# Performance work log

Hardware: AMD Instinct MI355X
Metric: run time of the kernel (lower is better)

Reference implementation:

```python
import jax, jax.numpy as jnp
import numpy as np

N_NODES = 100_000
N_EDGES = 1_600_000
NUM_GRAPHS = 512
D1, D2, D3, D5, NUM_CLASSES = 3, 50, 15, 10, 6
BN_EPS = 1e-5


def setup_inputs() -> dict:
    key = jax.random.key(0)
    ks = jax.random.split(key, 16)

    def w(k, shape):
        fan_in = shape[0]
        return jax.random.normal(k, shape, jnp.float32) / np.sqrt(fan_in).astype(np.float32)

    return {
        "x": jax.random.normal(ks[0], (N_NODES, D1), jnp.float32),
        "edge_attr": jax.random.normal(ks[1], (N_EDGES, D1), jnp.float32),
        # edge MLP: Lin(9,50) -> ReLU -> Lin(50,15)
        "edge_w1": w(ks[2], (3 * D1, D2)), "edge_b1": jnp.zeros((D2,), jnp.float32),
        "edge_w2": w(ks[3], (D2, D3)), "edge_b2": jnp.zeros((D3,), jnp.float32),
        # node MLP: Lin(18,50) -> ReLU -> Lin(50,15)
        "node_w1": w(ks[4], (D1 + D3, D2)), "node_b1": jnp.zeros((D2,), jnp.float32),
        "node_w2": w(ks[5], (D2, D3)), "node_b2": jnp.zeros((D3,), jnp.float32),
        # readout head
        "fc1_w": w(ks[6], (D3, D5)), "fc1_b": jnp.zeros((D5,), jnp.float32),
        "bn_gamma": jnp.ones((D5,), jnp.float32), "bn_beta": jnp.zeros((D5,), jnp.float32),
        "fc2_w": w(ks[7], (D5, NUM_CLASSES)), "fc2_b": jnp.zeros((NUM_CLASSES,), jnp.float32),
        # graph structure
        "edge_index": jax.random.randint(ks[8], (2, N_EDGES), 0, N_NODES, jnp.int32),
        "batch": jnp.sort(jax.random.randint(ks[9], (N_NODES,), 0, NUM_GRAPHS, jnp.int32)),
    }


def _segment_mean(vals, idx, num_segments):
    s = jax.ops.segment_sum(vals, idx, num_segments=num_segments)
    c = jax.ops.segment_sum(jnp.ones((vals.shape[0], 1), vals.dtype), idx,
                            num_segments=num_segments)
    return s / jnp.maximum(c, 1.0)


def reference(x, edge_attr,
              edge_w1, edge_b1, edge_w2, edge_b2,
              node_w1, node_b1, node_w2, node_b2,
              fc1_w, fc1_b, bn_gamma, bn_beta, fc2_w, fc2_b,
              edge_index, batch):
    row, col = edge_index[0], edge_index[1]
    # edge model: cat([x[row], x[col], edge_attr]) -> MLP  -> [E, D3]
    e_in = jnp.concatenate([x[row], x[col], edge_attr], axis=1)
    edge_attr2 = jax.nn.relu(e_in @ edge_w1 + edge_b1) @ edge_w2 + edge_b2
    # node model: cat([x[col], edge_attr2]) -> MLP -> scatter_mean over row
    n_in = jnp.concatenate([x[col], edge_attr2], axis=1)  # [E, D1+D3]
    msg = jax.nn.relu(n_in @ node_w1 + node_b1) @ node_w2 + node_b2  # [E, D3]
    x2 = _segment_mean(msg, row, x.shape[0])  # [N, D3]
    # global mean pool per graph -> [G, D3]
    u = _segment_mean(x2, batch, NUM_GRAPHS)
    # head: fc1 -> BatchNorm1d (batch stats) -> relu -> fc2 -> log_softmax
    h = u @ fc1_w + fc1_b
    mu = h.mean(axis=0)
    var = h.var(axis=0)  # biased, matches BN training normalization
    h = bn_gamma * (h - mu) * jax.lax.rsqrt(var + BN_EPS) + bn_beta
    h = jax.nn.relu(h)
    logits = h @ fc2_w + fc2_b
    return jax.nn.log_softmax(logits, axis=1)
```

## Files before the change

kernel.cpp:

```cpp
#include <hip/hip_runtime.h>
#include <hip/hip_bf16.h>
#include <math.h>

#define N_NODES    100000
#define N_EDGES    1600000
#define NUM_GRAPHS 512
#define D2 50
#define D3 15
#define D5 10
#define NCLS 6
#define BN_EPS 1e-5f

#define NBLK1 ((N_NODES + 1023) / 1024)

#define W_EW1T 0
#define W_EW2T 2560
#define W_NW1T 3712
#define W_NW2T 6272
#define W_TOTAL 7680

#define EDGE_BLOCKS 2500
#define EDGE_WAVES  (EDGE_BLOCKS * 4)
#define TILES32     (N_EDGES / 32)
#define EDGE_ITERS  (TILES32 / EDGE_WAVES)

typedef __attribute__((ext_vector_type(8))) short short8;
typedef __attribute__((ext_vector_type(4))) float float4_;
union BU { unsigned u[4]; short8 s; };
union FU { unsigned u; float f; };

__device__ __forceinline__ unsigned short f2bf(float f) {
    __hip_bfloat16 h = __float2bfloat16(f);
    union { __hip_bfloat16 h; unsigned short u; } c; c.h = h; return c.u;
}
__device__ __forceinline__ unsigned pkbf(float a, float b) {
    unsigned r;
    asm("v_cvt_pk_bf16_f32 %0, %1, %2" : "=v"(r) : "v"(a), "v"(b));
    return r;
}
__device__ __forceinline__ unsigned bp(int s4, unsigned v) {
    return (unsigned)__builtin_amdgcn_ds_bpermute(s4, (int)v);
}
__device__ __forceinline__ float lo16(unsigned u) { FU c; c.u = u << 16; return c.f; }
__device__ __forceinline__ float hi16(unsigned u) { FU c; c.u = u & 0xFFFF0000u; return c.f; }

__global__ __launch_bounds__(256) void prep_kernel(
    const float* __restrict__ ew1, const float* __restrict__ eb1,
    const float* __restrict__ ew2, const float* __restrict__ eb2,
    const float* __restrict__ nw1, const float* __restrict__ nb1,
    const float* __restrict__ nw2, const float* __restrict__ nb2,
    unsigned short* __restrict__ wh,
    const float* __restrict__ x, ushort4* __restrict__ x4b,
    const int* __restrict__ edge_index, int* __restrict__ counts)
{
    int gtid = blockIdx.x * 256 + threadIdx.x;
    int gsz = gridDim.x * 256;

    for (int i = gtid; i < W_TOTAL; i += gsz) {
        float v = 0.0f;
        if (i < W_EW2T) {
            int m = i / 40, k = i % 40;
            if (m < 50) {
                if (k < 3)                 v = ew1[k * 50 + m];
                else if (k == 3)           v = eb1[m];
                else if (k >= 4 && k < 7)  v = ew1[(k - 1) * 50 + m];
                else if (k >= 8 && k < 11) v = ew1[(k - 2) * 50 + m];
            }
        } else if (i < W_NW1T) {
            int j = i - W_EW2T; int m = j / 72, k = j % 72;
            if (m < 15) { if (k < 50) v = ew2[k * 15 + m]; else if (k == 50) v = eb2[m]; }
        } else if (i < W_NW2T) {
            int j = i - W_NW1T; int m = j / 40, k = j % 40;
            if (m < 50) {
                if (k < 15)                  v = nw1[(3 + k) * 50 + m];
                else if (k >= 16 && k < 19)  v = nw1[(k - 16) * 50 + m];
                else if (k == 19)            v = nb1[m];
            }
        } else if (i < 7424) {
            int j = i - W_NW2T; int m = j / 72, k = j % 72;
            if (m < 15) { if (k < 50) v = nw2[k * 15 + m]; else if (k == 50) v = nb2[m]; }
        }
        wh[i] = f2bf(v);
    }

    for (int n = gtid; n < N_NODES; n += gsz) {
        ushort4 v;
        v.x = f2bf(x[n * 3 + 0]); v.y = f2bf(x[n * 3 + 1]);
        v.z = f2bf(x[n * 3 + 2]); v.w = 0;
        x4b[n] = v;
    }

    for (int e = gtid; e < N_EDGES; e += gsz)
        atomicAdd(&counts[edge_index[e]], 1);
}

__global__ __launch_bounds__(1024) void scan_kernel(
    const int* __restrict__ counts, int* __restrict__ scanned,
    int* __restrict__ cursor, int* __restrict__ gctr)
{
    __shared__ int wsum[16], wofs[16];
    __shared__ int base;
    int i = blockIdx.x * 1024 + threadIdx.x;
    int lane = threadIdx.x & 63, wid = threadIdx.x >> 6;
    int v = (i < N_NODES) ? counts[i] : 0;
    int sc = v;
    #pragma unroll
    for (int off = 1; off < 64; off <<= 1) {
        int t = __shfl_up(sc, off);
        if (lane >= off) sc += t;
    }
    if (lane == 63) wsum[wid] = sc;
    __syncthreads();
    if (wid == 0) {
        int s = (lane < 16) ? wsum[lane] : 0;
        #pragma unroll
        for (int off = 1; off < 16; off <<= 1) {
            int t = __shfl_up(s, off);
            if (lane >= off) s += t;
        }
        if (lane < 16) wofs[lane] = s - wsum[lane];
    }
    __syncthreads();
    int incl = sc + wofs[wid];
    if (threadIdx.x == 1023) base = atomicAdd(gctr, incl);
    __syncthreads();
    int start = base + incl - v;
    if (i < N_NODES) { scanned[i] = start; cursor[i] = start; }
}

struct EIn { unsigned w0, w1, w2, w3, h0, h1; int pos; };

__device__ __forceinline__ EIn load_in(int ebase, int n, int quad,
    const int* __restrict__ edge_index, const ushort4* __restrict__ x4b,
    const float* __restrict__ edge_attr, int* __restrict__ cursor)
{
    EIn r; r.w0 = r.w1 = r.w2 = r.w3 = 0; r.h0 = r.h1 = 0; r.pos = 0;
    int e = ebase + n;
    if (quad == 0) {
        int row = edge_index[e];
        int col = edge_index[N_EDGES + e];
        ushort4 xr = x4b[row];
        ushort4 xc = x4b[col];
        r.w0 = (unsigned)xr.x | ((unsigned)xr.y << 16);
        r.w1 = (unsigned)xr.z | (0x3F80u << 16);
        r.w2 = (unsigned)xc.x | ((unsigned)xc.y << 16);
        r.w3 = (unsigned)xc.z;
        r.pos = atomicAdd(&cursor[row], 1);
    } else if (quad == 1) {
        r.w0 = pkbf(edge_attr[e * 3 + 0], edge_attr[e * 3 + 1]);
        r.w1 = pkbf(edge_attr[e * 3 + 2], 0.0f);
    } else if (quad == 2) {
        int col = edge_index[N_EDGES + e];
        ushort4 xc = x4b[col];
        r.h0 = (unsigned)xc.x | ((unsigned)xc.y << 16);
        r.h1 = (unsigned)xc.z | (0x3F80u << 16);
    }
    return r;
}

__device__ __forceinline__ void perm64(const unsigned U[4][2], int s0, int s1, bool hi,
                                       short8& Bc0, short8& Bc1)
{
    BU b0, b1;
    {
        unsigned a0 = bp(s0, U[0][0]), a1 = bp(s0, U[1][0]);
        unsigned a2 = bp(s0, U[0][1]), a3 = bp(s0, U[1][1]);
        unsigned a4 = bp(s1, U[0][0]), a5 = bp(s1, U[1][0]);
        unsigned a6 = bp(s1, U[0][1]), a7 = bp(s1, U[1][1]);
        b0.u[0] = hi ? a1 : a0;
        b0.u[1] = hi ? a3 : a2;
        b0.u[2] = hi ? a5 : a4;
        b0.u[3] = hi ? a7 : a6;
    }
    {
        unsigned a0 = bp(s0, U[2][0]), a1 = bp(s0, U[3][0]);
        unsigned a2 = bp(s0, U[2][1]), a3 = bp(s0, U[3][1]);
        unsigned a4 = bp(s1, U[2][0]), a5 = bp(s1, U[3][0]);
        unsigned a6 = bp(s1, U[2][1]), a7 = bp(s1, U[3][1]);
        b1.u[0] = hi ? a1 : a0;
        b1.u[1] = hi ? a3 : a2;
        b1.u[2] = hi ? a5 : a4;
        b1.u[3] = hi ? a7 : a6;
    }
    Bc0 = b0.s; Bc1 = b1.s;
}

__device__ __forceinline__ short8 perm16(const unsigned U2[2], int s0, int s1,
                                         int quad, unsigned h0, unsigned h1)
{
    BU d;
    d.u[0] = bp(s0, U2[0]);
    d.u[1] = bp(s0, U2[1]);
    d.u[2] = bp(s1, U2[0]);
    d.u[3] = bp(s1, U2[1]);
    if (quad == 2) { d.u[0] = h0; d.u[1] = h1; d.u[2] = 0; d.u[3] = 0; }
    else if (quad == 3) { d.u[0] = 0; d.u[1] = 0; d.u[2] = 0; d.u[3] = 0; }
    return d.s;
}

__global__ __launch_bounds__(256) void edge_mfma_kernel(
    const unsigned short* __restrict__ wh_g,
    const ushort4* __restrict__ x4b, const float* __restrict__ edge_attr,
    const int* __restrict__ edge_index,
    int* __restrict__ cursor, unsigned short* __restrict__ msgb)
{
    int tid = threadIdx.x, wave = tid >> 6, lane = tid & 63;
    int n = lane & 15, quad = lane >> 4;

    short8 A1[4], A3[4];
    #pragma unroll
    for (int t4 = 0; t4 < 4; t4++) {
        A1[t4] = *(const short8*)(wh_g + W_EW1T + (t4 * 16 + n) * 40 + quad * 8);
        A3[t4] = *(const short8*)(wh_g + W_NW1T + (t4 * 16 + n) * 40 + quad * 8);
    }
    short8 A2[2], A4[2];
    #pragma unroll
    for (int kc = 0; kc < 2; kc++) {
        A2[kc] = *(const short8*)(wh_g + W_EW2T + n * 72 + kc * 32 + quad * 8);
        A4[kc] = *(const short8*)(wh_g + W_NW2T + n * 72 + kc * 32 + quad * 8);
    }

    int s0 = ((quad & 1) * 32 + n) * 4;
    int s1 = s0 + 64;
    bool hi = (quad & 2) != 0;

    const float4_ Z0 = {0.f, 0.f, 0.f, 0.f};

    int t = blockIdx.x * 4 + wave;
    EIn cur0 = load_in(t * 32,      n, quad, edge_index, x4b, edge_attr, cursor);
    EIn cur1 = load_in(t * 32 + 16, n, quad, edge_index, x4b, edge_attr, cursor);

    for (int it = 0; it < EDGE_ITERS; it++) {
        int p0 = __shfl(cur0.pos, n);
        int p1 = __shfl(cur1.pos, n);

        int tn = t + EDGE_WAVES;
        EIn nx0, nx1;
        nx0.w0 = nx0.w1 = nx0.w2 = nx0.w3 = nx0.h0 = nx0.h1 = 0; nx0.pos = 0;
        nx1 = nx0;
        if (it + 1 < EDGE_ITERS) {
            nx0 = load_in(tn * 32,      n, quad, edge_index, x4b, edge_attr, cursor);
            nx1 = load_in(tn * 32 + 16, n, quad, edge_index, x4b, edge_attr, cursor);
        }

        BU t0, t1;
        t0.u[0] = cur0.w0; t0.u[1] = cur0.w1; t0.u[2] = cur0.w2; t0.u[3] = cur0.w3;
        t1.u[0] = cur1.w0; t1.u[1] = cur1.w1; t1.u[2] = cur1.w2; t1.u[3] = cur1.w3;
        short8 B1a = t0.s, B1b = t1.s;

        unsigned U1a[4][2], U1b[4][2];
        #pragma unroll
        for (int t4 = 0; t4 < 4; t4++) {
            float4_ za = __builtin_amdgcn_mfma_f32_16x16x32_bf16(A1[t4], B1a, Z0, 0, 0, 0);
            float4_ zb = __builtin_amdgcn_mfma_f32_16x16x32_bf16(A1[t4], B1b, Z0, 0, 0, 0);
            U1a[t4][0] = pkbf(fmaxf(za[0], 0.f), fmaxf(za[1], 0.f));
            U1a[t4][1] = pkbf(fmaxf(za[2], 0.f), fmaxf(za[3], 0.f));
            U1b[t4][0] = pkbf(fmaxf(zb[0], 0.f), fmaxf(zb[1], 0.f));
            U1b[t4][1] = pkbf(fmaxf(zb[2], 0.f), fmaxf(zb[3], 0.f));
        }

        short8 B2a0, B2a1, B2b0, B2b1;
        perm64(U1a, s0, s1, hi, B2a0, B2a1);
        perm64(U1b, s0, s1, hi, B2b0, B2b1);
        if (quad == 2) {
            BU fa, fb; fa.s = B2a1; fb.s = B2b1;
            fa.u[1] = (fa.u[1] & 0xFFFF0000u) | 0x3F80u;
            fb.u[1] = (fb.u[1] & 0xFFFF0000u) | 0x3F80u;
            B2a1 = fa.s; B2b1 = fb.s;
        }

        float4_ a2a = __builtin_amdgcn_mfma_f32_16x16x32_bf16(A2[0], B2a0, Z0, 0, 0, 0);
        float4_ a2b = __builtin_amdgcn_mfma_f32_16x16x32_bf16(A2[0], B2b0, Z0, 0, 0, 0);
        a2a = __builtin_amdgcn_mfma_f32_16x16x32_bf16(A2[1], B2a1, a2a, 0, 0, 0);
        a2b = __builtin_amdgcn_mfma_f32_16x16x32_bf16(A2[1], B2b1, a2b, 0, 0, 0);

        unsigned U2a[2] = { pkbf(a2a[0], a2a[1]), pkbf(a2a[2], a2a[3]) };
        unsigned U2b[2] = { pkbf(a2b[0], a2b[1]), pkbf(a2b[2], a2b[3]) };

        short8 B3a = perm16(U2a, s0, s1, quad, cur0.h0, cur0.h1);
        short8 B3b = perm16(U2b, s0, s1, quad, cur1.h0, cur1.h1);

        unsigned U3a[4][2], U3b[4][2];
        #pragma unroll
        for (int t4 = 0; t4 < 4; t4++) {
            float4_ za = __builtin_amdgcn_mfma_f32_16x16x32_bf16(A3[t4], B3a, Z0, 0, 0, 0);
            float4_ zb = __builtin_amdgcn_mfma_f32_16x16x32_bf16(A3[t4], B3b, Z0, 0, 0, 0);
            U3a[t4][0] = pkbf(fmaxf(za[0], 0.f), fmaxf(za[1], 0.f));
            U3a[t4][1] = pkbf(fmaxf(za[2], 0.f), fmaxf(za[3], 0.f));
            U3b[t4][0] = pkbf(fmaxf(zb[0], 0.f), fmaxf(zb[1], 0.f));
            U3b[t4][1] = pkbf(fmaxf(zb[2], 0.f), fmaxf(zb[3], 0.f));
        }

        short8 B4a0, B4a1, B4b0, B4b1;
        perm64(U3a, s0, s1, hi, B4a0, B4a1);
        perm64(U3b, s0, s1, hi, B4b0, B4b1);
        if (quad == 2) {
            BU fa, fb; fa.s = B4a1; fb.s = B4b1;
            fa.u[1] = (fa.u[1] & 0xFFFF0000u) | 0x3F80u;
            fb.u[1] = (fb.u[1] & 0xFFFF0000u) | 0x3F80u;
            B4a1 = fa.s; B4b1 = fb.s;
        }

        float4_ ma = __builtin_amdgcn_mfma_f32_16x16x32_bf16(A4[0], B4a0, Z0, 0, 0, 0);
        float4_ mb = __builtin_amdgcn_mfma_f32_16x16x32_bf16(A4[0], B4b0, Z0, 0, 0, 0);
        ma = __builtin_amdgcn_mfma_f32_16x16x32_bf16(A4[1], B4a1, ma, 0, 0, 0);
        mb = __builtin_amdgcn_mfma_f32_16x16x32_bf16(A4[1], B4b1, mb, 0, 0, 0);

        uint2 pa, pb;
        pa.x = pkbf(ma[0], ma[1]); pa.y = pkbf(ma[2], ma[3]);
        pb.x = pkbf(mb[0], mb[1]); pb.y = pkbf(mb[2], mb[3]);
        *(uint2*)(msgb + (size_t)p0 * 16 + quad * 4) = pa;
        *(uint2*)(msgb + (size_t)p1 * 16 + quad * 4) = pb;

        cur0 = nx0; cur1 = nx1; t = tn;
    }
}

__global__ __launch_bounds__(256) void gather_pool_kernel(
    const unsigned short* __restrict__ msgb, const int* __restrict__ scanned,
    const int* __restrict__ counts, const int* __restrict__ batch,
    float* __restrict__ gsum)
{
    __shared__ float acc[64 * 16];
    int n0 = blockIdx.x * 256;
    int n = n0 + threadIdx.x;

    float v[16];
    #pragma unroll
    for (int k = 0; k < 16; k++) v[k] = 0.0f;
    if (n < N_NODES) {
        int start = scanned[n];
        int deg = counts[n];
        const uint4* mp = (const uint4*)(msgb + (size_t)start * 16);
        int j = 0;
        for (; j + 4 <= deg; j += 4) {
            uint4 q0 = mp[2 * j + 0], q1 = mp[2 * j + 1];
            uint4 q2 = mp[2 * j + 2], q3 = mp[2 * j + 3];
            uint4 q4 = mp[2 * j + 4], q5 = mp[2 * j + 5];
            uint4 q6 = mp[2 * j + 6], q7 = mp[2 * j + 7];
            v[0]  += lo16(q0.x) + lo16(q2.x) + lo16(q4.x) + lo16(q6.x);
            v[1]  += hi16(q0.x) + hi16(q2.x) + hi16(q4.x) + hi16(q6.x);
            v[2]  += lo16(q0.y) + lo16(q2.y) + lo16(q4.y) + lo16(q6.y);
            v[3]  += hi16(q0.y) + hi16(q2.y) + hi16(q4.y) + hi16(q6.y);
            v[4]  += lo16(q0.z) + lo16(q2.z) + lo16(q4.z) + lo16(q6.z);
            v[5]  += hi16(q0.z) + hi16(q2.z) + hi16(q4.z) + hi16(q6.z);
            v[6]  += lo16(q0.w) + lo16(q2.w) + lo16(q4.w) + lo16(q6.w);
            v[7]  += hi16(q0.w) + hi16(q2.w) + hi16(q4.w) + hi16(q6.w);
            v[8]  += lo16(q1.x) + lo16(q3.x) + lo16(q5.x) + lo16(q7.x);
            v[9]  += hi16(q1.x) + hi16(q3.x) + hi16(q5.x) + hi16(q7.x);
            v[10] += lo16(q1.y) + lo16(q3.y) + lo16(q5.y) + lo16(q7.y);
            v[11] += hi16(q1.y) + hi16(q3.y) + hi16(q5.y) + hi16(q7.y);
            v[12] += lo16(q1.z) + lo16(q3.z) + lo16(q5.z) + lo16(q7.z);
            v[13] += hi16(q1.z) + hi16(q3.z) + hi16(q5.z) + hi16(q7.z);
            v[14] += lo16(q1.w) + lo16(q3.w) + lo16(q5.w) + lo16(q7.w);
        }
        for (; j < deg; j++) {
            uint4 qa = mp[2 * j + 0], qb = mp[2 * j + 1];
            v[0]  += lo16(qa.x); v[1]  += hi16(qa.x);
            v[2]  += lo16(qa.y); v[3]  += hi16(qa.y);
            v[4]  += lo16(qa.z); v[5]  += hi16(qa.z);
            v[6]  += lo16(qa.w); v[7]  += hi16(qa.w);
            v[8]  += lo16(qb.x); v[9]  += hi16(qb.x);
            v[10] += lo16(qb.y); v[11] += hi16(qb.y);
            v[12] += lo16(qb.z); v[13] += hi16(qb.z);
            v[14] += lo16(qb.w);
        }
        float inv = 1.0f / fmaxf((float)deg, 1.0f);
        #pragma unroll
        for (int k = 0; k < 15; k++) v[k] *= inv;
        v[15] = 1.0f;
    }

    int gmin = batch[n0];
    int gmax = batch[min(n0 + 255, N_NODES - 1)];
    int range = gmax - gmin + 1;
    if (range <= 64) {
        for (int t = threadIdx.x; t < range * 16; t += 256) acc[t] = 0.0f;
        __syncthreads();
        if (n < N_NODES) {
            int g = batch[n] - gmin;
            float* dst = &acc[g * 16];
            #pragma unroll
            for (int k = 0; k < 16; k++) atomicAdd(&dst[k], v[k]);
        }
        __syncthreads();
        for (int t = threadIdx.x; t < range * 16; t += 256) {
            float w = acc[t];
            if (w != 0.0f) atomicAdd(&gsum[(size_t)gmin * 16 + t], w);
        }
    } else {
        if (n < N_NODES) {
            int g = batch[n];
            float* dst = gsum + (size_t)g * 16;
            #pragma unroll
            for (int k = 0; k < 16; k++) atomicAdd(&dst[k], v[k]);
        }
    }
}

__global__ __launch_bounds__(512) void head_kernel(
    const float* __restrict__ gsum,
    const float* __restrict__ fc1w, const float* __restrict__ fc1b,
    const float* __restrict__ gamma, const float* __restrict__ beta,
    const float* __restrict__ fc2w, const float* __restrict__ fc2b,
    float* __restrict__ out)
{
    __shared__ float ssum[D5], ssq[D5], smu[D5], sistd[D5];
    int g = threadIdx.x;
    if (g < D5) { ssum[g] = 0.0f; ssq[g] = 0.0f; }
    __syncthreads();

    const float* src = gsum + (size_t)g * 16;
    float inv = 1.0f / fmaxf(src[15], 1.0f);
    float u[D3];
    #pragma unroll
    for (int k = 0; k < D3; k++) u[k] = src[k] * inv;

    float h[D5];
    #pragma unroll
    for (int c = 0; c < D5; c++) h[c] = fc1b[c];
    #pragma unroll
    for (int k = 0; k < D3; k++) {
        float v = u[k];
        #pragma unroll
        for (int c = 0; c < D5; c++) h[c] = fmaf(v, fc1w[k * D5 + c], h[c]);
    }

    int lane = threadIdx.x & 63;
    #pragma unroll
    for (int c = 0; c < D5; c++) {
        float v = h[c];
        float v2 = v * v;
        #pragma unroll
        for (int off = 32; off >= 1; off >>= 1) {
            v  += __shfl_xor(v,  off);
            v2 += __shfl_xor(v2, off);
        }
        if (lane == 0) { atomicAdd(&ssum[c], v); atomicAdd(&ssq[c], v2); }
    }
    __syncthreads();
    if (g < D5) {
        float mu = ssum[g] * (1.0f / NUM_GRAPHS);
        float var = ssq[g] * (1.0f / NUM_GRAPHS) - mu * mu;
        smu[g] = mu;
        sistd[g] = rsqrtf(var + BN_EPS);
    }
    __syncthreads();

    float hn[D5];
    #pragma unroll
    for (int c = 0; c < D5; c++) {
        float v = gamma[c] * (h[c] - smu[c]) * sistd[c] + beta[c];
        hn[c] = fmaxf(v, 0.0f);
    }

    float lg[NCLS];
    #pragma unroll
    for (int j = 0; j < NCLS; j++) lg[j] = fc2b[j];
    #pragma unroll
    for (int c = 0; c < D5; c++) {
        float v = hn[c];
        #pragma unroll
        for (int j = 0; j < NCLS; j++) lg[j] = fmaf(v, fc2w[c * NCLS + j], lg[j]);
    }

    float m = lg[0];
    #pragma unroll
    for (int j = 1; j < NCLS; j++) m = fmaxf(m, lg[j]);
    float se = 0.0f;
    #pragma unroll
    for (int j = 0; j < NCLS; j++) se += expf(lg[j] - m);
    float lse = logf(se);
    #pragma unroll
    for (int j = 0; j < NCLS; j++) out[g * NCLS + j] = lg[j] - m - lse;
}

extern "C" void kernel_launch(void* const* d_in, const int* in_sizes, int n_in,
                              void* d_out, int out_size, void* d_ws, size_t ws_size,
                              hipStream_t stream) {
    const float* x         = (const float*)d_in[0];
    const float* edge_attr = (const float*)d_in[1];
    const float* ew1  = (const float*)d_in[2];
    const float* eb1  = (const float*)d_in[3];
    const float* ew2  = (const float*)d_in[4];
    const float* eb2  = (const float*)d_in[5];
    const float* nw1  = (const float*)d_in[6];
    const float* nb1  = (const float*)d_in[7];
    const float* nw2  = (const float*)d_in[8];
    const float* nb2  = (const float*)d_in[9];
    const float* fc1w = (const float*)d_in[10];
    const float* fc1b = (const float*)d_in[11];
    const float* gamma= (const float*)d_in[12];
    const float* beta = (const float*)d_in[13];
    const float* fc2w = (const float*)d_in[14];
    const float* fc2b = (const float*)d_in[15];
    const int* edge_index = (const int*)d_in[16];
    const int* batch      = (const int*)d_in[17];

    char* p = (char*)d_ws;
    unsigned short* msgb = (unsigned short*)p; p += (size_t)N_EDGES * 16 * sizeof(unsigned short);
    int* counts  = (int*)p;            p += (size_t)N_NODES * sizeof(int);
    int* gctr    = (int*)p;            p += 4 * sizeof(int);
    int* scanned = (int*)p;            p += (size_t)N_NODES * sizeof(int);
    int* cursor  = (int*)p;            p += (size_t)N_NODES * sizeof(int);
    ushort4* x4b = (ushort4*)p;        p += (size_t)N_NODES * sizeof(ushort4);
    float* gsum  = (float*)p;          p += (size_t)NUM_GRAPHS * 16 * sizeof(float);
    unsigned short* wh = (unsigned short*)p; p += W_TOTAL * sizeof(unsigned short);

    hipMemsetAsync(counts, 0, (size_t)(N_NODES + 4) * sizeof(int), stream);
    hipMemsetAsync(gsum, 0, (size_t)NUM_GRAPHS * 16 * sizeof(float), stream);

    int egrid = (N_EDGES + 255) / 256;
    int ngrid = (N_NODES + 255) / 256;

    prep_kernel<<<egrid, 256, 0, stream>>>(
        ew1, eb1, ew2, eb2, nw1, nb1, nw2, nb2, wh,
        x, x4b, edge_index, counts);
    scan_kernel<<<NBLK1, 1024, 0, stream>>>(counts, scanned, cursor, gctr);
    edge_mfma_kernel<<<EDGE_BLOCKS, 256, 0, stream>>>(
        wh, x4b, edge_attr, edge_index, cursor, msgb);
    gather_pool_kernel<<<ngrid, 256, 0, stream>>>(
        msgb, scanned, counts, batch, gsum);
    head_kernel<<<1, 512, 0, stream>>>(
        gsum, fc1w, fc1b, gamma, beta, fc2w, fc2b, (float*)d_out);
}
```

Baseline: 312.5 us.

## Fuse edge MLP with per-graph pooling via 1/deg-weighted shared-memory accumulation

The change removes the CSR scan, the per-edge message buffer and the gather kernel. Each edge message is scaled by 1/deg(row) and added straight into a per-block shared-memory accumulator indexed by graph id, which works because the mean-of-means is linear. Per-block partials (1024×512×16 floats) are written out and summed by a new reduce kernel. Node counts per graph are now computed in prep through a shared histogram. This saves the write and read of the 51 MB bf16 message buffer and the scan launch. In exchange it adds many LDS float atomics per edge and roughly 32 MB of partial writes and reads.

```diff
diff --git a/kernel.cpp b/kernel.cpp
--- a/kernel.cpp
+++ b/kernel.cpp
@@ -11,23 +11,21 @@
 #define NCLS 6
 #define BN_EPS 1e-5f
 
-#define NBLK1 ((N_NODES + 1023) / 1024)
-
 #define W_EW1T 0
 #define W_EW2T 2560
 #define W_NW1T 3712
 #define W_NW2T 6272
 #define W_TOTAL 7680
 
-#define EDGE_BLOCKS 2500
+#define EDGE_BLOCKS 1024
 #define EDGE_WAVES  (EDGE_BLOCKS * 4)
 #define TILES32     (N_EDGES / 32)
-#define EDGE_ITERS  (TILES32 / EDGE_WAVES)
+
+#define GPAD 17
 
 typedef __attribute__((ext_vector_type(8))) short short8;
 typedef __attribute__((ext_vector_type(4))) float float4_;
 union BU { unsigned u[4]; short8 s; };
-union FU { unsigned u; float f; };
 
 __device__ __forceinline__ unsigned short f2bf(float f) {
     __hip_bfloat16 h = __float2bfloat16(f);
@@ -41,8 +39,6 @@
 __device__ __forceinline__ unsigned bp(int s4, unsigned v) {
     return (unsigned)__builtin_amdgcn_ds_bpermute(s4, (int)v);
 }
-__device__ __forceinline__ float lo16(unsigned u) { FU c; c.u = u << 16; return c.f; }
-__device__ __forceinline__ float hi16(unsigned u) { FU c; c.u = u & 0xFFFF0000u; return c.f; }
 
 __global__ __launch_bounds__(256) void prep_kernel(
     const float* __restrict__ ew1, const float* __restrict__ eb1,
@@ -51,10 +47,15 @@
     const float* __restrict__ nw2, const float* __restrict__ nb2,
     unsigned short* __restrict__ wh,
     const float* __restrict__ x, ushort4* __restrict__ x4b,
-    const int* __restrict__ edge_index, int* __restrict__ counts)
-{
+    const int* __restrict__ edge_index, int* __restrict__ counts,
+    const int* __restrict__ batch, float* __restrict__ gsum)
+{
+    __shared__ int bh[NUM_GRAPHS];
     int gtid = blockIdx.x * 256 + threadIdx.x;
     int gsz = gridDim.x * 256;
+
+    for (int i = threadIdx.x; i < NUM_GRAPHS; i += 256) bh[i] = 0;
+    __syncthreads();
 
     for (int i = gtid; i < W_TOTAL; i += gsz) {
         float v = 0.0f;
@@ -88,53 +89,27 @@
         v.x = f2bf(x[n * 3 + 0]); v.y = f2bf(x[n * 3 + 1]);
         v.z = f2bf(x[n * 3 + 2]); v.w = 0;
         x4b[n] = v;
+        atomicAdd(&bh[batch[n]], 1);
     }
 
     for (int e = gtid; e < N_EDGES; e += gsz)
         atomicAdd(&counts[edge_index[e]], 1);
-}
-
-__global__ __launch_bounds__(1024) void scan_kernel(
-    const int* __restrict__ counts, int* __restrict__ scanned,
-    int* __restrict__ cursor, int* __restrict__ gctr)
-{
-    __shared__ int wsum[16], wofs[16];
-    __shared__ int base;
-    int i = blockIdx.x * 1024 + threadIdx.x;
-    int lane = threadIdx.x & 63, wid = threadIdx.x >> 6;
-    int v = (i < N_NODES) ? counts[i] : 0;
-    int sc = v;
-    #pragma unroll
-    for (int off = 1; off < 64; off <<= 1) {
-        int t = __shfl_up(sc, off);
-        if (lane >= off) sc += t;
-    }
-    if (lane == 63) wsum[wid] = sc;
-    __syncthreads();
-    if (wid == 0) {
-        int s = (lane < 16) ? wsum[lane] : 0;
-        #pragma unroll
-        for (int off = 1; off < 16; off <<= 1) {
-            int t = __shfl_up(s, off);
-            if (lane >= off) s += t;
-        }
-        if (lane < 16) wofs[lane] = s - wsum[lane];
-    }
-    __syncthreads();
-    int incl = sc + wofs[wid];
-    if (threadIdx.x == 1023) base = atomicAdd(gctr, incl);
-    __syncthreads();
-    int start = base + incl - v;
-    if (i < N_NODES) { scanned[i] = start; cursor[i] = start; }
-}
-
-struct EIn { unsigned w0, w1, w2, w3, h0, h1; int pos; };
+
+    __syncthreads();
+    for (int i = threadIdx.x; i < NUM_GRAPHS; i += 256) {
+        int v = bh[i];
+        if (v) atomicAdd(&gsum[i * 16 + 15], (float)v);
+    }
+}
+
+struct EIn { unsigned w0, w1, w2, w3, h0, h1; int g; float invd; };
 
 __device__ __forceinline__ EIn load_in(int ebase, int n, int quad,
     const int* __restrict__ edge_index, const ushort4* __restrict__ x4b,
-    const float* __restrict__ edge_attr, int* __restrict__ cursor)
-{
-    EIn r; r.w0 = r.w1 = r.w2 = r.w3 = 0; r.h0 = r.h1 = 0; r.pos = 0;
+    const float* __restrict__ edge_attr,
+    const int* __restrict__ counts, const int* __restrict__ batch)
+{
+    EIn r; r.w0 = r.w1 = r.w2 = r.w3 = 0; r.h0 = r.h1 = 0; r.g = 0; r.invd = 0.0f;
     int e = ebase + n;
     if (quad == 0) {
         int row = edge_index[e];
@@ -145,7 +120,8 @@
         r.w1 = (unsigned)xr.z | (0x3F80u << 16);
         r.w2 = (unsigned)xc.x | ((unsigned)xc.y << 16);
         r.w3 = (unsigned)xc.z;
-        r.pos = atomicAdd(&cursor[row], 1);
+        r.g = batch[row];
+        r.invd = 1.0f / (float)counts[row];
     } else if (quad == 1) {
         r.w0 = pkbf(edge_attr[e * 3 + 0], edge_attr[e * 3 + 1]);
         r.w1 = pkbf(edge_attr[e * 3 + 2], 0.0f);
@@ -198,14 +174,19 @@
     return d.s;
 }
 
-__global__ __launch_bounds__(256) void edge_mfma_kernel(
+__global__ __launch_bounds__(256) void edge_fused_kernel(
     const unsigned short* __restrict__ wh_g,
     const ushort4* __restrict__ x4b, const float* __restrict__ edge_attr,
     const int* __restrict__ edge_index,
-    int* __restrict__ cursor, unsigned short* __restrict__ msgb)
-{
+    const int* __restrict__ counts, const int* __restrict__ batch,
+    float* __restrict__ partial)
+{
+    __shared__ float acc[NUM_GRAPHS * GPAD];
     int tid = threadIdx.x, wave = tid >> 6, lane = tid & 63;
     int n = lane & 15, quad = lane >> 4;
+
+    for (int i = tid; i < NUM_GRAPHS * GPAD; i += 256) acc[i] = 0.0f;
+    __syncthreads();
 
     short8 A1[4], A3[4];
     #pragma unroll
@@ -227,20 +208,23 @@
     const float4_ Z0 = {0.f, 0.f, 0.f, 0.f};
 
     int t = blockIdx.x * 4 + wave;
-    EIn cur0 = load_in(t * 32,      n, quad, edge_index, x4b, edge_attr, cursor);
-    EIn cur1 = load_in(t * 32 + 16, n, quad, edge_index, x4b, edge_attr, cursor);
-
-    for (int it = 0; it < EDGE_ITERS; it++) {
-        int p0 = __shfl(cur0.pos, n);
-        int p1 = __shfl(cur1.pos, n);
+    EIn cur0 = load_in(t * 32,      n, quad, edge_index, x4b, edge_attr, counts, batch);
+    EIn cur1 = load_in(t * 32 + 16, n, quad, edge_index, x4b, edge_attr, counts, batch);
+
+    for (;;) {
+        int g0 = __shfl(cur0.g, n);
+        float q0 = __shfl(cur0.invd, n);
+        int g1 = __shfl(cur1.g, n);
+        float q1 = __shfl(cur1.invd, n);
 
         int tn = t + EDGE_WAVES;
+        bool more = (tn < TILES32);
         EIn nx0, nx1;
-        nx0.w0 = nx0.w1 = nx0.w2 = nx0.w3 = nx0.h0 = nx0.h1 = 0; nx0.pos = 0;
+        nx0.w0 = nx0.w1 = nx0.w2 = nx0.w3 = nx0.h0 = nx0.h1 = 0; nx0.g = 0; nx0.invd = 0.f;
         nx1 = nx0;
-        if (it + 1 < EDGE_ITERS) {
-            nx0 = load_in(tn * 32,      n, quad, edge_index, x4b, edge_attr, cursor);
-            nx1 = load_in(tn * 32 + 16, n, quad, edge_index, x4b, edge_attr, cursor);
+        if (more) {
+            nx0 = load_in(tn * 32,      n, quad, edge_index, x4b, edge_attr, counts, batch);
+            nx1 = load_in(tn * 32 + 16, n, quad, edge_index, x4b, edge_attr, counts, batch);
         }
 
         BU t0, t1;
@@ -306,95 +290,46 @@
         ma = __builtin_amdgcn_mfma_f32_16x16x32_bf16(A4[1], B4a1, ma, 0, 0, 0);
         mb = __builtin_amdgcn_mfma_f32_16x16x32_bf16(A4[1], B4b1, mb, 0, 0, 0);
 
-        uint2 pa, pb;
-        pa.x = pkbf(ma[0], ma[1]); pa.y = pkbf(ma[2], ma[3]);
-        pb.x = pkbf(mb[0], mb[1]); pb.y = pkbf(mb[2], mb[3]);
-        *(uint2*)(msgb + (size_t)p0 * 16 + quad * 4) = pa;
-        *(uint2*)(msgb + (size_t)p1 * 16 + quad * 4) = pb;
-
+        float* a0 = &acc[g0 * GPAD + quad * 4];
+        float* a1 = &acc[g1 * GPAD + quad * 4];
+        atomicAdd(&a0[0], ma[0] * q0);
+        atomicAdd(&a0[1], ma[1] * q0);
+        atomicAdd(&a0[2], ma[2] * q0);
+        atomicAdd(&a1[0], mb[0] * q1);
+        atomicAdd(&a1[1], mb[1] * q1);
+        atomicAdd(&a1[2], mb[2] * q1);
+        if (quad != 3) {
+            atomicAdd(&a0[3], ma[3] * q0);
+            atomicAdd(&a1[3], mb[3] * q1);
+        }
+
+        if (!more) break;
         cur0 = nx0; cur1 = nx1; t = tn;
     }
-}
-
-__global__ __launch_bounds__(256) void gather_pool_kernel(
-    const unsigned short* __restrict__ msgb, const int* __restrict__ scanned,
-    const int* __restrict__ counts, const int* __restrict__ batch,
-    float* __restrict__ gsum)
-{
-    __shared__ float acc[64 * 16];
-    int n0 = blockIdx.x * 256;
-    int n = n0 + threadIdx.x;
-
-    float v[16];
-    #pragma unroll
-    for (int k = 0; k < 16; k++) v[k] = 0.0f;
-    if (n < N_NODES) {
-        int start = scanned[n];
-        int deg = counts[n];
-        const uint4* mp = (const uint4*)(msgb + (size_t)start * 16);
-        int j = 0;
-        for (; j + 4 <= deg; j += 4) {
-            uint4 q0 = mp[2 * j + 0], q1 = mp[2 * j + 1];
-            uint4 q2 = mp[2 * j + 2], q3 = mp[2 * j + 3];
-            uint4 q4 = mp[2 * j + 4], q5 = mp[2 * j + 5];
-            uint4 q6 = mp[2 * j + 6], q7 = mp[2 * j + 7];
-            v[0]  += lo16(q0.x) + lo16(q2.x) + lo16(q4.x) + lo16(q6.x);
-            v[1]  += hi16(q0.x) + hi16(q2.x) + hi16(q4.x) + hi16(q6.x);
-            v[2]  += lo16(q0.y) + lo16(q2.y) + lo16(q4.y) + lo16(q6.y);
-            v[3]  += hi16(q0.y) + hi16(q2.y) + hi16(q4.y) + hi16(q6.y);
-            v[4]  += lo16(q0.z) + lo16(q2.z) + lo16(q4.z) + lo16(q6.z);
-            v[5]  += hi16(q0.z) + hi16(q2.z) + hi16(q4.z) + hi16(q6.z);
-            v[6]  += lo16(q0.w) + lo16(q2.w) + lo16(q4.w) + lo16(q6.w);
-            v[7]  += hi16(q0.w) + hi16(q2.w) + hi16(q4.w) + hi16(q6.w);
-            v[8]  += lo16(q1.x) + lo16(q3.x) + lo16(q5.x) + lo16(q7.x);
-            v[9]  += hi16(q1.x) + hi16(q3.x) + hi16(q5.x) + hi16(q7.x);
-            v[10] += lo16(q1.y) + lo16(q3.y) + lo16(q5.y) + lo16(q7.y);
-            v[11] += hi16(q1.y) + hi16(q3.y) + hi16(q5.y) + hi16(q7.y);
-            v[12] += lo16(q1.z) + lo16(q3.z) + lo16(q5.z) + lo16(q7.z);
-            v[13] += hi16(q1.z) + hi16(q3.z) + hi16(q5.z) + hi16(q7.z);
-            v[14] += lo16(q1.w) + lo16(q3.w) + lo16(q5.w) + lo16(q7.w);
-        }
-        for (; j < deg; j++) {
-            uint4 qa = mp[2 * j + 0], qb = mp[2 * j + 1];
-            v[0]  += lo16(qa.x); v[1]  += hi16(qa.x);
-            v[2]  += lo16(qa.y); v[3]  += hi16(qa.y);
-            v[4]  += lo16(qa.z); v[5]  += hi16(qa.z);
-            v[6]  += lo16(qa.w); v[7]  += hi16(qa.w);
-            v[8]  += lo16(qb.x); v[9]  += hi16(qb.x);
-            v[10] += lo16(qb.y); v[11] += hi16(qb.y);
-            v[12] += lo16(qb.z); v[13] += hi16(qb.z);
-            v[14] += lo16(qb.w);
-        }
-        float inv = 1.0f / fmaxf((float)deg, 1.0f);
-        #pragma unroll
-        for (int k = 0; k < 15; k++) v[k] *= inv;
-        v[15] = 1.0f;
-    }
-
-    int gmin = batch[n0];
-    int gmax = batch[min(n0 + 255, N_NODES - 1)];
-    int range = gmax - gmin + 1;
-    if (range <= 64) {
-        for (int t = threadIdx.x; t < range * 16; t += 256) acc[t] = 0.0f;
-        __syncthreads();
-        if (n < N_NODES) {
-            int g = batch[n] - gmin;
-            float* dst = &acc[g * 16];
-            #pragma unroll
-            for (int k = 0; k < 16; k++) atomicAdd(&dst[k], v[k]);
-        }
-        __syncthreads();
-        for (int t = threadIdx.x; t < range * 16; t += 256) {
-            float w = acc[t];
-            if (w != 0.0f) atomicAdd(&gsum[(size_t)gmin * 16 + t], w);
-        }
-    } else {
-        if (n < N_NODES) {
-            int g = batch[n];
-            float* dst = gsum + (size_t)g * 16;
-            #pragma unroll
-            for (int k = 0; k < 16; k++) atomicAdd(&dst[k], v[k]);
-        }
+
+    __syncthreads();
+    float* pb = partial + (size_t)blockIdx.x * (NUM_GRAPHS * 16);
+    for (int i = tid; i < NUM_GRAPHS * 16; i += 256)
+        pb[i] = acc[(i >> 4) * GPAD + (i & 15)];
+}
+
+__global__ __launch_bounds__(256) void reduce_kernel(
+    const float* __restrict__ partial, float* __restrict__ gsum)
+{
+    __shared__ float red[256];
+    int g = blockIdx.x;
+    float s = 0.0f;
+    for (int j = threadIdx.x; j < EDGE_BLOCKS * 16; j += 256) {
+        int b = j >> 4, c = j & 15;
+        s += partial[(size_t)b * (NUM_GRAPHS * 16) + g * 16 + c];
+    }
+    red[threadIdx.x] = s;
+    __syncthreads();
+    if (threadIdx.x < 16) {
+        float t = 0.0f;
+        #pragma unroll
+        for (int k = 0; k < 16; k++) t += red[k * 16 + threadIdx.x];
+        gsum[g * 16 + threadIdx.x] += t;
     }
 }
 
@@ -498,29 +433,23 @@
     const int* batch      = (const int*)d_in[17];
 
     char* p = (char*)d_ws;
-    unsigned short* msgb = (unsigned short*)p; p += (size_t)N_EDGES * 16 * sizeof(unsigned short);
+    float* partial = (float*)p;        p += (size_t)EDGE_BLOCKS * NUM_GRAPHS * 16 * sizeof(float);
     int* counts  = (int*)p;            p += (size_t)N_NODES * sizeof(int);
-    int* gctr    = (int*)p;            p += 4 * sizeof(int);
-    int* scanned = (int*)p;            p += (size_t)N_NODES * sizeof(int);
-    int* cursor  = (int*)p;            p += (size_t)N_NODES * sizeof(int);
     ushort4* x4b = (ushort4*)p;        p += (size_t)N_NODES * sizeof(ushort4);
     float* gsum  = (float*)p;          p += (size_t)NUM_GRAPHS * 16 * sizeof(float);
     unsigned short* wh = (unsigned short*)p; p += W_TOTAL * sizeof(unsigned short);
 
-    hipMemsetAsync(counts, 0, (size_t)(N_NODES + 4) * sizeof(int), stream);
+    hipMemsetAsync(counts, 0, (size_t)N_NODES * sizeof(int), stream);
     hipMemsetAsync(gsum, 0, (size_t)NUM_GRAPHS * 16 * sizeof(float), stream);
 
     int egrid = (N_EDGES + 255) / 256;
-    int ngrid = (N_NODES + 255) / 256;
 
     prep_kernel<<<egrid, 256, 0, stream>>>(
         ew1, eb1, ew2, eb2, nw1, nb1, nw2, nb2, wh,
-        x, x4b, edge_index, counts);
-    scan_kernel<<<NBLK1, 1024, 0, stream>>>(counts, scanned, cursor, gctr);
-    edge_mfma_kernel<<<EDGE_BLOCKS, 256, 0, stream>>>(
-        wh, x4b, edge_attr, edge_index, cursor, msgb);
-    gather_pool_kernel<<<ngrid, 256, 0, stream>>>(
-        msgb, scanned, counts, batch, gsum);
+        x, x4b, edge_index, counts, batch, gsum);
+    edge_fused_kernel<<<EDGE_BLOCKS, 256, 0, stream>>>(
+        wh, x4b, edge_attr, edge_index, counts, batch, partial);
+    reduce_kernel<<<NUM_GRAPHS, 256, 0, stream>>>(partial, gsum);
     head_kernel<<<1, 512, 0, stream>>>(
         gsum, fc1w, fc1b, gamma, beta, fc2w, fc2b, (float*)d_out);
 }
```

New measurement: 382.2 us. 22.3% more time.
